# Kernel tuning notes

Hardware: AMD Instinct MI355X
Metric: run time of the kernel (lower is better)

Reference implementation:

```python
import jax, jax.numpy as jnp
import numpy as np

N, E, D, H, C = 50000, 1600000, 128, 2, 32

def setup_inputs() -> dict:
    key = jax.random.key(0)
    ks = jax.random.split(key, 8)
    x = jax.random.normal(ks[0], (N, D), jnp.float32)
    edge_index = jax.random.randint(ks[1], (2, E), 0, N)
    intra_enrichment_weights = jax.random.uniform(ks[2], (E,), jnp.float32)
    W = jax.random.normal(ks[3], (D, H * C), jnp.float32) * (1.0 / np.sqrt(D))
    att_src = jax.random.normal(ks[4], (H, C), jnp.float32) * 0.1
    att_dst = jax.random.normal(ks[5], (H, C), jnp.float32) * 0.1
    bias = jnp.zeros((H * C,), jnp.float32)
    enrichment_scale = jnp.asarray(0.01, jnp.float32)
    return dict(x=x, edge_index=edge_index,
                intra_enrichment_weights=intra_enrichment_weights,
                W=W, att_src=att_src, att_dst=att_dst, bias=bias,
                enrichment_scale=enrichment_scale)

def reference(x, edge_index, intra_enrichment_weights, W, att_src, att_dst, bias, enrichment_scale):
    n = x.shape[0]
    xf = jax.nn.elu(x)                       # F.elu on input features
    h = (xf @ W).reshape(n, H, C)            # [N, heads, out]
    # GATConv default add_self_loops=True
    loop = jnp.arange(n, dtype=edge_index.dtype)
    src = jnp.concatenate([edge_index[0], loop])
    dst = jnp.concatenate([edge_index[1], loop])
    a_src = jnp.einsum('nhc,hc->nh', h, att_src)   # [N, H]
    a_dst = jnp.einsum('nhc,hc->nh', h, att_dst)
    alpha = jax.nn.leaky_relu(a_src[src] + a_dst[dst], 0.2)  # [E+N, H]
    # softmax over incoming edges per destination node
    m = jax.ops.segment_max(alpha, dst, num_segments=n)
    e = jnp.exp(alpha - m[dst])
    denom = jax.ops.segment_sum(e, dst, num_segments=n)
    p = e / denom[dst]                       # every node has a self-loop -> denom > 0
    out = jax.ops.segment_sum(h[src] * p[:, :, None], dst, num_segments=n)  # [N, H, C]
    out = out.reshape(n, H * C) + bias
    # enrichment bias (scatter-mean of per-edge weights over source nodes)
    s0 = edge_index[0]
    nw = jax.ops.segment_sum(intra_enrichment_weights, s0, num_segments=n)
    cnt = jax.ops.segment_sum(jnp.ones_like(intra_enrichment_weights), s0, num_segments=n)
    nw = nw / jnp.maximum(cnt, 1.0)
    nw = jnp.clip(nw, 0.2, 5.0)
    scale_factor = 0.1 * jax.nn.sigmoid(enrichment_scale)
    return out + scale_factor * (nw[:, None] - 1.0)
```

## Files before the change

### kernel.cpp

```cpp
#include <hip/hip_runtime.h>


typedef unsigned int u32;
typedef unsigned short u16;

#define SLOTS2 2624
#define NB2_MAX 800
#define EPB 4096

#define XS 136
#define CS 68

#define SMEM_F 34816

typedef __attribute__((ext_vector_type(8))) short short8;
typedef __attribute__((ext_vector_type(4))) float float4v;

__device__ __forceinline__ u16 f2bf(float f) {
    union { float f; u32 u; } v; v.f = f;
    u32 r = v.u + 0x7fffu + ((v.u >> 16) & 1u);
    return (u16)(r >> 16);
}
__device__ __forceinline__ float bf2f(u16 u) {
    union { u32 i; float f; } v; v.i = ((u32)u) << 16; return v.f;
}
__device__ __forceinline__ float bf_lo(u32 u) {
    union { u32 i; float f; } v; v.i = u << 16; return v.f;
}
__device__ __forceinline__ float bf_hi(u32 u) {
    union { u32 i; float f; } v; v.i = u & 0xFFFF0000u; return v.f;
}
__device__ __forceinline__ void bf_split(float v, short& hi, short& lo) {
    u16 h = f2bf(v);
    float hf = bf2f(h);
    hi = (short)h;
    lo = (short)f2bf(v - hf);
}

__global__ void k_prep(const float* __restrict__ Wm,
                       short* __restrict__ Whf, short* __restrict__ Wlf,
                       int* cursA, int* cursB)
{
    int t = threadIdx.x;
    for (int i = t; i < NB2_MAX; i += 256) { cursA[i] = 0; cursB[i] = 0; }
    for (int p = t; p < 1024; p += 256) {
        int frag = p >> 6, l = p & 63;
        int ks = frag >> 2, nt = frag & 3;
        int q = l >> 4, m = l & 15;
        int f = nt * 16 + m;
#pragma unroll
        for (int j = 0; j < 8; ++j) {
            int k = ks * 32 + q * 8 + j;
            float wv = Wm[k * 64 + f];
            short hi, lo; bf_split(wv, hi, lo);
            Whf[p * 8 + j] = hi;
            Wlf[p * 8 + j] = lo;
        }
    }
}

static __device__ __forceinline__ void node_body(
    char* smem, int nb_id,
    const float* __restrict__ x,
    const short* __restrict__ Whf, const short* __restrict__ Wlf,
    const float* __restrict__ att_s, const float* __restrict__ att_d,
    u32* __restrict__ hb32, float* __restrict__ a_src, float* __restrict__ a_dst,
    int nN)
{
    short* Ah = (short*)smem;
    short* Al = (short*)(smem + 17408);
    float* Cl = (float*)Ah;

    int t = threadIdx.x;
    int n0 = nb_id * 64;

    for (int j = 0; j < 8; ++j) {
        int idx = t + 256 * j;
        int r = idx >> 5, c4 = idx & 31;
        int gn = n0 + r;
        float4 xv = make_float4(0.f, 0.f, 0.f, 0.f);
        if (gn < nN) xv = ((const float4*)x)[(size_t)gn * 32 + c4];
        float e[4];
        e[0] = xv.x > 0.f ? xv.x : __expf(xv.x) - 1.f;
        e[1] = xv.y > 0.f ? xv.y : __expf(xv.y) - 1.f;
        e[2] = xv.z > 0.f ? xv.z : __expf(xv.z) - 1.f;
        e[3] = xv.w > 0.f ? xv.w : __expf(xv.w) - 1.f;
        short h4[4], l4[4];
#pragma unroll
        for (int i = 0; i < 4; ++i) bf_split(e[i], h4[i], l4[i]);
        *(short4*)&Ah[r * XS + c4 * 4] = make_short4(h4[0], h4[1], h4[2], h4[3]);
        *(short4*)&Al[r * XS + c4 * 4] = make_short4(l4[0], l4[1], l4[2], l4[3]);
    }
    __syncthreads();

    {
        int w = t >> 6, l = t & 63;
        int q = l >> 4, m = l & 15;
        int arow = w * 16 + m;
        float4v acc[4] = {};
#pragma unroll
        for (int ks = 0; ks < 4; ++ks) {
            int k0 = ks * 32 + q * 8;
            short8 ah = *(const short8*)&Ah[arow * XS + k0];
            short8 al = *(const short8*)&Al[arow * XS + k0];
#pragma unroll
            for (int nt = 0; nt < 4; ++nt) {
                short8 bh = *(const short8*)&Whf[((ks * 4 + nt) * 64 + l) * 8];
                short8 bl = *(const short8*)&Wlf[((ks * 4 + nt) * 64 + l) * 8];
                acc[nt] = __builtin_amdgcn_mfma_f32_16x16x32_bf16(ah, bh, acc[nt], 0, 0, 0);
                acc[nt] = __builtin_amdgcn_mfma_f32_16x16x32_bf16(ah, bl, acc[nt], 0, 0, 0);
                acc[nt] = __builtin_amdgcn_mfma_f32_16x16x32_bf16(al, bh, acc[nt], 0, 0, 0);
            }
        }
        __syncthreads();
#pragma unroll
        for (int nt = 0; nt < 4; ++nt)
#pragma unroll
            for (int r = 0; r < 4; ++r)
                Cl[(w * 16 + q * 4 + r) * CS + nt * 16 + m] = acc[nt][r];
    }
    __syncthreads();

    {
        int nl = t >> 2, fq = t & 3;
        int gn = n0 + nl;
        float ps = 0.f, pd = 0.f;
        if (gn < nN) {
            float hv[16];
#pragma unroll
            for (int i = 0; i < 16; ++i) {
                int f = fq * 16 + i;
                hv[i] = Cl[nl * CS + f];
                ps = fmaf(hv[i], att_s[f], ps);
                pd = fmaf(hv[i], att_d[f], pd);
            }
#pragma unroll
            for (int i = 0; i < 8; ++i) {
                u32 pk = ((u32)f2bf(hv[2 * i + 1]) << 16) | (u32)f2bf(hv[2 * i]);
                hb32[(size_t)gn * 32 + fq * 8 + i] = pk;
            }
        }
        float ps2 = ps + __shfl_xor(ps, 1, 64);
        float pd2 = pd + __shfl_xor(pd, 1, 64);
        if (gn < nN && (fq & 1) == 0) {
            a_src[2 * gn + (fq >> 1)] = ps2;
            a_dst[2 * gn + (fq >> 1)] = pd2;
        }
    }
}

static __device__ __forceinline__ void sort_body(
    char* smem, int pa_id, int sideB,
    const int* __restrict__ ei, const float* __restrict__ wgt,
    int* curs, u32* buf, int E, int nb2)
{
    u32* arr  = (u32*)smem;
    int* cnt  = (int*)(smem + 16384);
    int* lofs = (int*)(smem + 19584);
    int* bas  = (int*)(smem + 22784);
    int* part = (int*)(smem + 25984);

    int t = threadIdx.x;
    int base = pa_id * EPB;
    int nv = min(EPB, E - base);
    int key[16]; u32 pay[16];
#pragma unroll
    for (int k = 0; k < 16; ++k) {
        int e = base + k * 256 + t;
        if (e < E) {
            if (sideB) {
                key[k] = ei[e];
                u32 wq = (u32)(wgt[e] * 65536.f);
                if (wq > 0xFFFFu) wq = 0xFFFFu;
                pay[k] = wq;
            } else {
                key[k] = ei[E + e];
                pay[k] = (u32)ei[e];
            }
        } else { key[k] = -1; pay[k] = 0u; }
    }

    for (int b = t; b < nb2; b += 256) cnt[b] = 0;
    __syncthreads();
#pragma unroll
    for (int k = 0; k < 16; ++k)
        if (key[k] >= 0) atomicAdd(&cnt[key[k] >> 6], 1);
    __syncthreads();
    for (int b = t; b < nb2; b += 256) {
        int c = cnt[b];
        if (c > 0) bas[b] = atomicAdd(&curs[b], c);
    }
    __syncthreads();
    {
        int c[4]; int s = 0;
#pragma unroll
        for (int i = 0; i < 4; ++i) {
            int bb = 4 * t + i;
            c[i] = (bb < nb2) ? cnt[bb] : 0;
            s += c[i];
        }
        part[t] = s;
        __syncthreads();
        for (int off = 1; off < 256; off <<= 1) {
            int v = (t >= off) ? part[t - off] : 0;
            __syncthreads();
            part[t] += v;
            __syncthreads();
        }
        int excl = part[t] - s;
#pragma unroll
        for (int i = 0; i < 4; ++i) {
            int bb = 4 * t + i;
            if (bb < nb2) lofs[bb] = excl;
            excl += c[i];
        }
    }
    __syncthreads();
    for (int b = t; b < nb2; b += 256) cnt[b] = 0;
    __syncthreads();
#pragma unroll
    for (int k = 0; k < 16; ++k) {
        if (key[k] >= 0) {
            int bk = key[k] >> 6;
            int r = lofs[bk] + atomicAdd(&cnt[bk], 1);
            arr[r] = ((u32)bk << 22) | ((u32)(key[k] & 63) << 16) | pay[k];
        }
    }
    __syncthreads();
    for (int i = t; i < nv; i += 256) {
        u32 va = arr[i];
        int bk = va >> 22;
        int g = bas[bk] + (i - lofs[bk]);
        if (g < SLOTS2) buf[(size_t)bk * SLOTS2 + g] = va & 0x3FFFFFu;
    }
}

__global__ __launch_bounds__(256) void k_fused(
    const float* __restrict__ x,
    const short* __restrict__ Whf, const short* __restrict__ Wlf,
    const float* __restrict__ att_s, const float* __restrict__ att_d,
    u32* __restrict__ hb32, float* __restrict__ a_src, float* __restrict__ a_dst,
    const int* __restrict__ ei, const float* __restrict__ wgt,
    int* cursA, int* cursB, u32* bufA, u32* bufB,
    int E, int nb2, int nblkA, int nN)
{
    __shared__ __align__(16) char smem[SMEM_F];
    int bid = blockIdx.x;
    int g = bid >> 2, r = bid & 3;
    if (g < nblkA && r == 0) {
        sort_body(smem, g, 0, ei, wgt, cursA, bufA, E, nb2);
    } else if (g < nblkA && r == 2) {
        sort_body(smem, g, 1, ei, wgt, cursB, bufB, E, nb2);
    } else {
        int sortBefore = (g < nblkA) ? (2 * g + (r >= 1 ? 1 : 0) + (r >= 3 ? 1 : 0))
                                     : 2 * nblkA;
        node_body(smem, bid - sortBefore, x, Whf, Wlf, att_s, att_d,
                  hb32, a_src, a_dst, nN);
    }
}

__global__ __launch_bounds__(512) void k_final(
    const u32* __restrict__ hb32,
    const float* __restrict__ a_src, const float* __restrict__ a_dst,
    const u32* __restrict__ bufA, const int* __restrict__ cursA,
    const u32* __restrict__ bufB, const int* __restrict__ cursB,
    const float* __restrict__ bias, const float* __restrict__ esc,
    float* __restrict__ out, int nN)
{
    __shared__ u32 st[SLOTS2];
    __shared__ u16 st2[SLOTS2];
    __shared__ int ldeg[64], lscan[64], lcur[64];
    __shared__ int usum[64], ucnt[64];

    int b = blockIdx.x, t = threadIdx.x;
    int n0 = b << 6;
    int nA = cursA[b]; if (nA > SLOTS2) nA = SLOTS2;
    int nB = cursB[b]; if (nB > SLOTS2) nB = SLOTS2;

    if (t < 64) { ldeg[t] = 0; lcur[t] = 0; usum[t] = 0; ucnt[t] = 0; }
    __syncthreads();
    for (int i = t; i < nA; i += 512) {
        u32 v = bufA[(size_t)b * SLOTS2 + i];
        st[i] = v;
        atomicAdd(&ldeg[v >> 16], 1);
    }
    for (int i = t; i < nB; i += 512) {
        u32 v = bufB[(size_t)b * SLOTS2 + i];
        atomicAdd(&usum[v >> 16], (int)(v & 0xFFFFu));
        atomicAdd(&ucnt[v >> 16], 1);
    }
    __syncthreads();
    if (t < 64) lscan[t] = ldeg[t];
    __syncthreads();
    for (int off = 1; off < 64; off <<= 1) {
        int v = 0;
        if (t < 64 && t >= off) v = lscan[t - off];
        __syncthreads();
        if (t < 64) lscan[t] += v;
        __syncthreads();
    }
    if (t < 64) lscan[t] -= ldeg[t];
    __syncthreads();
    for (int i = t; i < nA; i += 512) {
        u32 v = st[i];
        int dl = v >> 16;
        int pos = lscan[dl] + atomicAdd(&lcur[dl], 1);
        st2[pos] = (u16)(v & 0xFFFFu);
    }
    __syncthreads();

    int ws = t >> 6, lane = t & 63;
    int q = lane >> 4, fl = lane & 15, head = fl >> 3;
    const uint2* hb2 = (const uint2*)hb32;
    float escv = esc[0];
    float sf = 0.1f / (1.f + __expf(-escv));
    float4 bb = ((const float4*)bias)[fl];

    for (int dl0 = ws; dl0 < 64; dl0 += 16) {
        int dlA = dl0, dlB = dl0 + 8;
        int gnA = n0 + dlA, gnB = n0 + dlB;
        if (gnA >= nN) break;
        bool vB = (gnB < nN);

        int begA = lscan[dlA], cntA = ldeg[dlA];
        float2 advA = ((const float2*)a_dst)[gnA];
        float2 asvA = ((const float2*)a_src)[gnA];
        float tA0 = asvA.x + advA.x; tA0 = tA0 > 0.f ? tA0 : 0.2f * tA0;
        float tA1 = asvA.y + advA.y; tA1 = tA1 > 0.f ? tA1 : 0.2f * tA1;
        float esA0 = __expf(tA0), esA1 = __expf(tA1);
        float aA0 = 0.f, aA1 = 0.f, aA2 = 0.f, aA3 = 0.f;
        if (q == 0) {
            float eself = head ? esA1 : esA0;
            uint2 hs = hb2[(size_t)gnA * 16 + fl];
            aA0 = eself * bf_lo(hs.x); aA1 = eself * bf_hi(hs.x);
            aA2 = eself * bf_lo(hs.y); aA3 = eself * bf_hi(hs.y);
        }
        float dsA = 0.f;

        int begB = 0, cntB = 0;
        float2 advB = make_float2(0.f, 0.f);
        float esB0 = 0.f, esB1 = 0.f;
        float aB0 = 0.f, aB1 = 0.f, aB2 = 0.f, aB3 = 0.f;
        float dsB = 0.f;
        if (vB) {
            begB = lscan[dlB]; cntB = ldeg[dlB];
            advB = ((const float2*)a_dst)[gnB];
            float2 asvB = ((const float2*)a_src)[gnB];
            float tB0 = asvB.x + advB.x; tB0 = tB0 > 0.f ? tB0 : 0.2f * tB0;
            float tB1 = asvB.y + advB.y; tB1 = tB1 > 0.f ? tB1 : 0.2f * tB1;
            esB0 = __expf(tB0); esB1 = __expf(tB1);
            if (q == 0) {
                float eself = head ? esB1 : esB0;
                uint2 hs = hb2[(size_t)gnB * 16 + fl];
                aB0 = eself * bf_lo(hs.x); aB1 = eself * bf_hi(hs.x);
                aB2 = eself * bf_lo(hs.y); aB3 = eself * bf_hi(hs.y);
            }
        }

        int nwA = (cntA + 63) >> 6, nwB = (cntB + 63) >> 6;
        int nwin = nwA > nwB ? nwA : nwB;
        for (int w = 0; w < nwin; ++w) {
            int b0 = w << 6;
            u32 siA = (u32)gnA; float eA0 = 0.f, eA1 = 0.f; int wnA = 0;
            if (w < nwA) {
                wnA = cntA - b0; if (wnA > 64) wnA = 64;
                if (lane < wnA) {
                    siA = (u32)st2[begA + b0 + lane];
                    float2 ap = ((const float2*)a_src)[siA];
                    float v0 = ap.x + advA.x; v0 = v0 > 0.f ? v0 : 0.2f * v0;
                    float v1 = ap.y + advA.y; v1 = v1 > 0.f ? v1 : 0.2f * v1;
                    eA0 = __expf(v0); eA1 = __expf(v1);
                }
            }
            u32 siB = (u32)gnA; float eB0 = 0.f, eB1 = 0.f; int wnB = 0;
            if (w < nwB) {
                wnB = cntB - b0; if (wnB > 64) wnB = 64;
                if (lane < wnB) {
                    siB = (u32)st2[begB + b0 + lane];
                    float2 ap = ((const float2*)a_src)[siB];
                    float v0 = ap.x + advB.x; v0 = v0 > 0.f ? v0 : 0.2f * v0;
                    float v1 = ap.y + advB.y; v1 = v1 > 0.f ? v1 : 0.2f * v1;
                    eB0 = __expf(v0); eB1 = __expf(v1);
                }
            }
            int wmax = wnA > wnB ? wnA : wnB;
            int iters = (wmax + 3) >> 2;
#pragma unroll 4
            for (int k = 0; k < iters; ++k) {
                int e = 4 * k + q;
                u32 rsiA = __shfl(siA, e, 64);
                u32 rsiB = __shfl(siB, e, 64);
                uint2 hvA = hb2[(size_t)rsiA * 16 + fl];
                uint2 hvB = hb2[(size_t)rsiB * 16 + fl];
                float w0A = __shfl(eA0, e, 64), w1A = __shfl(eA1, e, 64);
                float w0B = __shfl(eB0, e, 64), w1B = __shfl(eB1, e, 64);
                float wA = head ? w1A : w0A;
                float wB = head ? w1B : w0B;
                dsA += wA; dsB += wB;
                aA0 = fmaf(wA, bf_lo(hvA.x), aA0);
                aA1 = fmaf(wA, bf_hi(hvA.x), aA1);
                aA2 = fmaf(wA, bf_lo(hvA.y), aA2);
                aA3 = fmaf(wA, bf_hi(hvA.y), aA3);
                aB0 = fmaf(wB, bf_lo(hvB.x), aB0);
                aB1 = fmaf(wB, bf_hi(hvB.x), aB1);
                aB2 = fmaf(wB, bf_lo(hvB.y), aB2);
                aB3 = fmaf(wB, bf_hi(hvB.y), aB3);
            }
        }
        dsA += __shfl_xor(dsA, 16, 64); dsA += __shfl_xor(dsA, 32, 64);
        dsB += __shfl_xor(dsB, 16, 64); dsB += __shfl_xor(dsB, 32, 64);
        aA0 += __shfl_xor(aA0, 16, 64); aA0 += __shfl_xor(aA0, 32, 64);
        aA1 += __shfl_xor(aA1, 16, 64); aA1 += __shfl_xor(aA1, 32, 64);
        aA2 += __shfl_xor(aA2, 16, 64); aA2 += __shfl_xor(aA2, 32, 64);
        aA3 += __shfl_xor(aA3, 16, 64); aA3 += __shfl_xor(aA3, 32, 64);
        aB0 += __shfl_xor(aB0, 16, 64); aB0 += __shfl_xor(aB0, 32, 64);
        aB1 += __shfl_xor(aB1, 16, 64); aB1 += __shfl_xor(aB1, 32, 64);
        aB2 += __shfl_xor(aB2, 16, 64); aB2 += __shfl_xor(aB2, 32, 64);
        aB3 += __shfl_xor(aB3, 16, 64); aB3 += __shfl_xor(aB3, 32, 64);

        if (q == 0) {
            {
                float den = (head ? esA1 : esA0) + dsA;
                float inv = 1.f / den;
                float cntf = (float)ucnt[dlA];
                float nw = ((float)usum[dlA] * (1.f / 65536.f)) / fmaxf(cntf, 1.f);
                nw = fminf(fmaxf(nw, 0.2f), 5.f);
                float en = sf * (nw - 1.f);
                float4 o;
                o.x = aA0 * inv + bb.x + en;
                o.y = aA1 * inv + bb.y + en;
                o.z = aA2 * inv + bb.z + en;
                o.w = aA3 * inv + bb.w + en;
                ((float4*)out)[(size_t)gnA * 16 + fl] = o;
            }
            if (vB) {
                float den = (head ? esB1 : esB0) + dsB;
                float inv = 1.f / den;
                float cntf = (float)ucnt[dlB];
                float nw = ((float)usum[dlB] * (1.f / 65536.f)) / fmaxf(cntf, 1.f);
                nw = fminf(fmaxf(nw, 0.2f), 5.f);
                float en = sf * (nw - 1.f);
                float4 o;
                o.x = aB0 * inv + bb.x + en;
                o.y = aB1 * inv + bb.y + en;
                o.z = aB2 * inv + bb.z + en;
                o.w = aB3 * inv + bb.w + en;
                ((float4*)out)[(size_t)gnB * 16 + fl] = o;
            }
        }
    }
}

extern "C" void kernel_launch(void* const* d_in, const int* in_sizes, int n_in,
                              void* d_out, int out_size, void* d_ws, size_t ws_size,
                              hipStream_t stream)
{
    const float* x     = (const float*)d_in[0];
    const int*   ei    = (const int*)d_in[1];
    const float* wgt   = (const float*)d_in[2];
    const float* Wm    = (const float*)d_in[3];
    const float* att_s = (const float*)d_in[4];
    const float* att_d = (const float*)d_in[5];
    const float* bias  = (const float*)d_in[6];
    const float* esc   = (const float*)d_in[7];
    float* out = (float*)d_out;

    int nN = in_sizes[0] / 128;
    int E  = in_sizes[2];
    int NB2 = (nN + 63) / 64;

    char* p = (char*)d_ws;
    auto alloc = [&](size_t bytes) -> char* {
        char* r = p; p += (bytes + 255) & ~(size_t)255; return r;
    };
    u32*   hb32  = (u32*)  alloc((size_t)nN * 32 * 4);
    float* a_src = (float*)alloc((size_t)nN * 2 * 4);
    float* a_dst = (float*)alloc((size_t)nN * 2 * 4);
    short* Whf   = (short*)alloc(16 * 64 * 8 * 2);
    short* Wlf   = (short*)alloc(16 * 64 * 8 * 2);
    int*   cursA = (int*)  alloc(NB2_MAX * 4);
    int*   cursB = (int*)  alloc(NB2_MAX * 4);
    u32*   bufA  = (u32*)  alloc((size_t)NB2 * SLOTS2 * 4);
    u32*   bufB  = (u32*)  alloc((size_t)NB2 * SLOTS2 * 4);

    int nblkA = (E + EPB - 1) / EPB;
    int nblkN = (nN + 63) / 64;
    int nblkF = 2 * nblkA + nblkN;

    k_prep<<<dim3(1), dim3(256), 0, stream>>>(Wm, Whf, Wlf, cursA, cursB);
    k_fused<<<dim3(nblkF), dim3(256), 0, stream>>>(x, Whf, Wlf, att_s, att_d,
                                                   hb32, a_src, a_dst,
                                                   ei, wgt, cursA, cursB, bufA, bufB,
                                                   E, NB2, nblkA, nN);
    k_final<<<dim3(NB2), dim3(512), 0, stream>>>(hb32, a_src, a_dst, bufA, cursA,
                                                 bufB, cursB, bias, esc, out, nN);
}
```

Measured before the change: 170.4 us.

## Process four destination nodes per wave in final kernel and drop staging buffer

Each wave in the final aggregation kernel now interleaves four destination nodes instead of two, which puts more independent gathers in flight and hides memory latency. The shared-memory staging array is removed and the bucket buffer is re-read from global memory in the second pass, which cuts LDS usage. Launch bounds now request 6 blocks per CU. The wider interleave raises register pressure and does more wasted padded iterations when node degrees differ, and the second global read adds traffic.

```diff
diff --git a/kernel.cpp b/kernel.cpp
--- a/kernel.cpp
+++ b/kernel.cpp
@@ -259,7 +259,7 @@
     }
 }
 
-__global__ __launch_bounds__(512) void k_final(
+__global__ __launch_bounds__(512, 6) void k_final(
     const u32* __restrict__ hb32,
     const float* __restrict__ a_src, const float* __restrict__ a_dst,
     const u32* __restrict__ bufA, const int* __restrict__ cursA,
@@ -267,7 +267,6 @@
     const float* __restrict__ bias, const float* __restrict__ esc,
     float* __restrict__ out, int nN)
 {
-    __shared__ u32 st[SLOTS2];
     __shared__ u16 st2[SLOTS2];
     __shared__ int ldeg[64], lscan[64], lcur[64];
     __shared__ int usum[64], ucnt[64];
@@ -281,7 +280,6 @@
     __syncthreads();
     for (int i = t; i < nA; i += 512) {
         u32 v = bufA[(size_t)b * SLOTS2 + i];
-        st[i] = v;
         atomicAdd(&ldeg[v >> 16], 1);
     }
     for (int i = t; i < nB; i += 512) {
@@ -302,7 +300,7 @@
     if (t < 64) lscan[t] -= ldeg[t];
     __syncthreads();
     for (int i = t; i < nA; i += 512) {
-        u32 v = st[i];
+        u32 v = bufA[(size_t)b * SLOTS2 + i];
         int dl = v >> 16;
         int pos = lscan[dl] + atomicAdd(&lcur[dl], 1);
         st2[pos] = (u16)(v & 0xFFFFu);
@@ -316,136 +314,107 @@
     float sf = 0.1f / (1.f + __expf(-escv));
     float4 bb = ((const float4*)bias)[fl];
 
-    for (int dl0 = ws; dl0 < 64; dl0 += 16) {
-        int dlA = dl0, dlB = dl0 + 8;
-        int gnA = n0 + dlA, gnB = n0 + dlB;
-        if (gnA >= nN) break;
-        bool vB = (gnB < nN);
-
-        int begA = lscan[dlA], cntA = ldeg[dlA];
-        float2 advA = ((const float2*)a_dst)[gnA];
-        float2 asvA = ((const float2*)a_src)[gnA];
-        float tA0 = asvA.x + advA.x; tA0 = tA0 > 0.f ? tA0 : 0.2f * tA0;
-        float tA1 = asvA.y + advA.y; tA1 = tA1 > 0.f ? tA1 : 0.2f * tA1;
-        float esA0 = __expf(tA0), esA1 = __expf(tA1);
-        float aA0 = 0.f, aA1 = 0.f, aA2 = 0.f, aA3 = 0.f;
-        if (q == 0) {
-            float eself = head ? esA1 : esA0;
-            uint2 hs = hb2[(size_t)gnA * 16 + fl];
-            aA0 = eself * bf_lo(hs.x); aA1 = eself * bf_hi(hs.x);
-            aA2 = eself * bf_lo(hs.y); aA3 = eself * bf_hi(hs.y);
-        }
-        float dsA = 0.f;
-
-        int begB = 0, cntB = 0;
-        float2 advB = make_float2(0.f, 0.f);
-        float esB0 = 0.f, esB1 = 0.f;
-        float aB0 = 0.f, aB1 = 0.f, aB2 = 0.f, aB3 = 0.f;
-        float dsB = 0.f;
-        if (vB) {
-            begB = lscan[dlB]; cntB = ldeg[dlB];
-            advB = ((const float2*)a_dst)[gnB];
-            float2 asvB = ((const float2*)a_src)[gnB];
-            float tB0 = asvB.x + advB.x; tB0 = tB0 > 0.f ? tB0 : 0.2f * tB0;
-            float tB1 = asvB.y + advB.y; tB1 = tB1 > 0.f ? tB1 : 0.2f * tB1;
-            esB0 = __expf(tB0); esB1 = __expf(tB1);
-            if (q == 0) {
-                float eself = head ? esB1 : esB0;
-                uint2 hs = hb2[(size_t)gnB * 16 + fl];
-                aB0 = eself * bf_lo(hs.x); aB1 = eself * bf_hi(hs.x);
-                aB2 = eself * bf_lo(hs.y); aB3 = eself * bf_hi(hs.y);
-            }
-        }
-
-        int nwA = (cntA + 63) >> 6, nwB = (cntB + 63) >> 6;
-        int nwin = nwA > nwB ? nwA : nwB;
+    for (int j = 0; j < 2; ++j) {
+        int dlb = ws + 32 * j;
+        int gn4[4], beg4[4], cnt4[4];
+        float adx[4], ady[4], e0s[4], e1s[4], ds4[4];
+        float ac0[4], ac1[4], ac2[4], ac3[4];
+        bool val[4];
+#pragma unroll
+        for (int c = 0; c < 4; ++c) {
+            int dl = dlb + 8 * c;
+            int g = n0 + dl;
+            gn4[c] = g;
+            val[c] = (g < nN);
+            beg4[c] = lscan[dl];
+            cnt4[c] = val[c] ? ldeg[dl] : 0;
+            float2 adv = make_float2(0.f, 0.f), asv = make_float2(0.f, 0.f);
+            if (val[c]) {
+                adv = ((const float2*)a_dst)[g];
+                asv = ((const float2*)a_src)[g];
+            }
+            adx[c] = adv.x; ady[c] = adv.y;
+            float t0 = asv.x + adv.x; t0 = t0 > 0.f ? t0 : 0.2f * t0;
+            float t1 = asv.y + adv.y; t1 = t1 > 0.f ? t1 : 0.2f * t1;
+            e0s[c] = __expf(t0); e1s[c] = __expf(t1);
+            ac0[c] = ac1[c] = ac2[c] = ac3[c] = 0.f;
+            ds4[c] = 0.f;
+            if (q == 0 && val[c]) {
+                float eself = head ? e1s[c] : e0s[c];
+                uint2 hs = hb2[(size_t)g * 16 + fl];
+                ac0[c] = eself * bf_lo(hs.x);
+                ac1[c] = eself * bf_hi(hs.x);
+                ac2[c] = eself * bf_lo(hs.y);
+                ac3[c] = eself * bf_hi(hs.y);
+            }
+        }
+        int nwin = 0;
+#pragma unroll
+        for (int c = 0; c < 4; ++c) {
+            int nw = (cnt4[c] + 63) >> 6;
+            if (nw > nwin) nwin = nw;
+        }
         for (int w = 0; w < nwin; ++w) {
             int b0 = w << 6;
-            u32 siA = (u32)gnA; float eA0 = 0.f, eA1 = 0.f; int wnA = 0;
-            if (w < nwA) {
-                wnA = cntA - b0; if (wnA > 64) wnA = 64;
-                if (lane < wnA) {
-                    siA = (u32)st2[begA + b0 + lane];
-                    float2 ap = ((const float2*)a_src)[siA];
-                    float v0 = ap.x + advA.x; v0 = v0 > 0.f ? v0 : 0.2f * v0;
-                    float v1 = ap.y + advA.y; v1 = v1 > 0.f ? v1 : 0.2f * v1;
-                    eA0 = __expf(v0); eA1 = __expf(v1);
+            u32 si4[4]; float we0[4], we1[4]; int wn4[4];
+#pragma unroll
+            for (int c = 0; c < 4; ++c) {
+                si4[c] = (u32)n0; we0[c] = 0.f; we1[c] = 0.f; wn4[c] = 0;
+                if (b0 < cnt4[c]) {
+                    int wn = cnt4[c] - b0; if (wn > 64) wn = 64;
+                    wn4[c] = wn;
+                    if (lane < wn) {
+                        si4[c] = (u32)st2[beg4[c] + b0 + lane];
+                        float2 ap = ((const float2*)a_src)[si4[c]];
+                        float v0 = ap.x + adx[c]; v0 = v0 > 0.f ? v0 : 0.2f * v0;
+                        float v1 = ap.y + ady[c]; v1 = v1 > 0.f ? v1 : 0.2f * v1;
+                        we0[c] = __expf(v0); we1[c] = __expf(v1);
+                    }
                 }
             }
-            u32 siB = (u32)gnA; float eB0 = 0.f, eB1 = 0.f; int wnB = 0;
-            if (w < nwB) {
-                wnB = cntB - b0; if (wnB > 64) wnB = 64;
-                if (lane < wnB) {
-                    siB = (u32)st2[begB + b0 + lane];
-                    float2 ap = ((const float2*)a_src)[siB];
-                    float v0 = ap.x + advB.x; v0 = v0 > 0.f ? v0 : 0.2f * v0;
-                    float v1 = ap.y + advB.y; v1 = v1 > 0.f ? v1 : 0.2f * v1;
-                    eB0 = __expf(v0); eB1 = __expf(v1);
-                }
-            }
-            int wmax = wnA > wnB ? wnA : wnB;
+            int wmax = 0;
+#pragma unroll
+            for (int c = 0; c < 4; ++c) if (wn4[c] > wmax) wmax = wn4[c];
             int iters = (wmax + 3) >> 2;
-#pragma unroll 4
+#pragma unroll 2
             for (int k = 0; k < iters; ++k) {
                 int e = 4 * k + q;
-                u32 rsiA = __shfl(siA, e, 64);
-                u32 rsiB = __shfl(siB, e, 64);
-                uint2 hvA = hb2[(size_t)rsiA * 16 + fl];
-                uint2 hvB = hb2[(size_t)rsiB * 16 + fl];
-                float w0A = __shfl(eA0, e, 64), w1A = __shfl(eA1, e, 64);
-                float w0B = __shfl(eB0, e, 64), w1B = __shfl(eB1, e, 64);
-                float wA = head ? w1A : w0A;
-                float wB = head ? w1B : w0B;
-                dsA += wA; dsB += wB;
-                aA0 = fmaf(wA, bf_lo(hvA.x), aA0);
-                aA1 = fmaf(wA, bf_hi(hvA.x), aA1);
-                aA2 = fmaf(wA, bf_lo(hvA.y), aA2);
-                aA3 = fmaf(wA, bf_hi(hvA.y), aA3);
-                aB0 = fmaf(wB, bf_lo(hvB.x), aB0);
-                aB1 = fmaf(wB, bf_hi(hvB.x), aB1);
-                aB2 = fmaf(wB, bf_lo(hvB.y), aB2);
-                aB3 = fmaf(wB, bf_hi(hvB.y), aB3);
-            }
-        }
-        dsA += __shfl_xor(dsA, 16, 64); dsA += __shfl_xor(dsA, 32, 64);
-        dsB += __shfl_xor(dsB, 16, 64); dsB += __shfl_xor(dsB, 32, 64);
-        aA0 += __shfl_xor(aA0, 16, 64); aA0 += __shfl_xor(aA0, 32, 64);
-        aA1 += __shfl_xor(aA1, 16, 64); aA1 += __shfl_xor(aA1, 32, 64);
-        aA2 += __shfl_xor(aA2, 16, 64); aA2 += __shfl_xor(aA2, 32, 64);
-        aA3 += __shfl_xor(aA3, 16, 64); aA3 += __shfl_xor(aA3, 32, 64);
-        aB0 += __shfl_xor(aB0, 16, 64); aB0 += __shfl_xor(aB0, 32, 64);
-        aB1 += __shfl_xor(aB1, 16, 64); aB1 += __shfl_xor(aB1, 32, 64);
-        aB2 += __shfl_xor(aB2, 16, 64); aB2 += __shfl_xor(aB2, 32, 64);
-        aB3 += __shfl_xor(aB3, 16, 64); aB3 += __shfl_xor(aB3, 32, 64);
-
-        if (q == 0) {
-            {
-                float den = (head ? esA1 : esA0) + dsA;
+#pragma unroll
+                for (int c = 0; c < 4; ++c) {
+                    u32 rsi = __shfl(si4[c], e, 64);
+                    uint2 hv = hb2[(size_t)rsi * 16 + fl];
+                    float w0 = __shfl(we0[c], e, 64);
+                    float w1 = __shfl(we1[c], e, 64);
+                    float wv = head ? w1 : w0;
+                    ds4[c] += wv;
+                    ac0[c] = fmaf(wv, bf_lo(hv.x), ac0[c]);
+                    ac1[c] = fmaf(wv, bf_hi(hv.x), ac1[c]);
+                    ac2[c] = fmaf(wv, bf_lo(hv.y), ac2[c]);
+                    ac3[c] = fmaf(wv, bf_hi(hv.y), ac3[c]);
+                }
+            }
+        }
+#pragma unroll
+        for (int c = 0; c < 4; ++c) {
+            ds4[c] += __shfl_xor(ds4[c], 16, 64); ds4[c] += __shfl_xor(ds4[c], 32, 64);
+            ac0[c] += __shfl_xor(ac0[c], 16, 64); ac0[c] += __shfl_xor(ac0[c], 32, 64);
+            ac1[c] += __shfl_xor(ac1[c], 16, 64); ac1[c] += __shfl_xor(ac1[c], 32, 64);
+            ac2[c] += __shfl_xor(ac2[c], 16, 64); ac2[c] += __shfl_xor(ac2[c], 32, 64);
+            ac3[c] += __shfl_xor(ac3[c], 16, 64); ac3[c] += __shfl_xor(ac3[c], 32, 64);
+            if (q == 0 && val[c]) {
+                int dl = dlb + 8 * c;
+                float den = (head ? e1s[c] : e0s[c]) + ds4[c];
                 float inv = 1.f / den;
-                float cntf = (float)ucnt[dlA];
-                float nw = ((float)usum[dlA] * (1.f / 65536.f)) / fmaxf(cntf, 1.f);
+                float cntf = (float)ucnt[dl];
+                float nw = ((float)usum[dl] * (1.f / 65536.f)) / fmaxf(cntf, 1.f);
                 nw = fminf(fmaxf(nw, 0.2f), 5.f);
                 float en = sf * (nw - 1.f);
                 float4 o;
-                o.x = aA0 * inv + bb.x + en;
-                o.y = aA1 * inv + bb.y + en;
-                o.z = aA2 * inv + bb.z + en;
-                o.w = aA3 * inv + bb.w + en;
-                ((float4*)out)[(size_t)gnA * 16 + fl] = o;
-            }
-            if (vB) {
-                float den = (head ? esB1 : esB0) + dsB;
-                float inv = 1.f / den;
-                float cntf = (float)ucnt[dlB];
-                float nw = ((float)usum[dlB] * (1.f / 65536.f)) / fmaxf(cntf, 1.f);
-                nw = fminf(fmaxf(nw, 0.2f), 5.f);
-                float en = sf * (nw - 1.f);
-                float4 o;
-                o.x = aB0 * inv + bb.x + en;
-                o.y = aB1 * inv + bb.y + en;
-                o.z = aB2 * inv + bb.z + en;
-                o.w = aB3 * inv + bb.w + en;
-                ((float4*)out)[(size_t)gnB * 16 + fl] = o;
+                o.x = ac0[c] * inv + bb.x + en;
+                o.y = ac1[c] * inv + bb.y + en;
+                o.z = ac2[c] * inv + bb.z + en;
+                o.w = ac3[c] * inv + bb.w + en;
+                ((float4*)out)[(size_t)gn4[c] * 16 + fl] = o;
             }
         }
     }
```

Result: slower. 200.4 us (+17.6%).

## Fuse prep, sort/node and final stages into one cooperative persistent kernel

Applied to the files above, without the earlier changes.

Replaces the three separate launches with a single cooperative kernel sized to full occupancy. Grid-wide syncs separate the phases, and atomic work counters hand out virtual blocks dynamically. The final stage now runs with 256 threads and shared memory carved from the common buffer, with a different node-to-wave assignment. The aim is to remove launch gaps and kernel-boundary drains. In exchange it adds grid.sync costs, atomic work-fetch overhead and possibly lower occupancy for the final phase, and it keeps the old three-kernel path as a fallback.

```diff
diff --git a/kernel.cpp b/kernel.cpp
--- a/kernel.cpp
+++ b/kernel.cpp
@@ -1,5 +1,8 @@
 #include <hip/hip_runtime.h>
-
+#include <hip/hip_cooperative_groups.h>
+
+
+namespace cg = cooperative_groups;
 
 typedef unsigned int u32;
 typedef unsigned short u16;
@@ -35,28 +38,6 @@
     float hf = bf2f(h);
     hi = (short)h;
     lo = (short)f2bf(v - hf);
-}
-
-__global__ void k_prep(const float* __restrict__ Wm,
-                       short* __restrict__ Whf, short* __restrict__ Wlf,
-                       int* cursA, int* cursB)
-{
-    int t = threadIdx.x;
-    for (int i = t; i < NB2_MAX; i += 256) { cursA[i] = 0; cursB[i] = 0; }
-    for (int p = t; p < 1024; p += 256) {
-        int frag = p >> 6, l = p & 63;
-        int ks = frag >> 2, nt = frag & 3;
-        int q = l >> 4, m = l & 15;
-        int f = nt * 16 + m;
-#pragma unroll
-        for (int j = 0; j < 8; ++j) {
-            int k = ks * 32 + q * 8 + j;
-            float wv = Wm[k * 64 + f];
-            short hi, lo; bf_split(wv, hi, lo);
-            Whf[p * 8 + j] = hi;
-            Wlf[p * 8 + j] = lo;
-        }
-    }
 }
 
 static __device__ __forceinline__ void node_body(
@@ -235,56 +216,36 @@
     }
 }
 
-__global__ __launch_bounds__(256) void k_fused(
-    const float* __restrict__ x,
-    const short* __restrict__ Whf, const short* __restrict__ Wlf,
-    const float* __restrict__ att_s, const float* __restrict__ att_d,
-    u32* __restrict__ hb32, float* __restrict__ a_src, float* __restrict__ a_dst,
-    const int* __restrict__ ei, const float* __restrict__ wgt,
-    int* cursA, int* cursB, u32* bufA, u32* bufB,
-    int E, int nb2, int nblkA, int nN)
-{
-    __shared__ __align__(16) char smem[SMEM_F];
-    int bid = blockIdx.x;
-    int g = bid >> 2, r = bid & 3;
-    if (g < nblkA && r == 0) {
-        sort_body(smem, g, 0, ei, wgt, cursA, bufA, E, nb2);
-    } else if (g < nblkA && r == 2) {
-        sort_body(smem, g, 1, ei, wgt, cursB, bufB, E, nb2);
-    } else {
-        int sortBefore = (g < nblkA) ? (2 * g + (r >= 1 ? 1 : 0) + (r >= 3 ? 1 : 0))
-                                     : 2 * nblkA;
-        node_body(smem, bid - sortBefore, x, Whf, Wlf, att_s, att_d,
-                  hb32, a_src, a_dst, nN);
-    }
-}
-
-__global__ __launch_bounds__(512) void k_final(
+static __device__ __forceinline__ void final_body(
+    char* smem, int b,
     const u32* __restrict__ hb32,
     const float* __restrict__ a_src, const float* __restrict__ a_dst,
     const u32* __restrict__ bufA, const int* __restrict__ cursA,
     const u32* __restrict__ bufB, const int* __restrict__ cursB,
-    const float* __restrict__ bias, const float* __restrict__ esc,
+    const float* __restrict__ bias, float sf,
     float* __restrict__ out, int nN)
 {
-    __shared__ u32 st[SLOTS2];
-    __shared__ u16 st2[SLOTS2];
-    __shared__ int ldeg[64], lscan[64], lcur[64];
-    __shared__ int usum[64], ucnt[64];
-
-    int b = blockIdx.x, t = threadIdx.x;
+    u32* st   = (u32*)smem;
+    u16* st2  = (u16*)(smem + 10496);
+    int* ldeg = (int*)(smem + 15744);
+    int* lscan= (int*)(smem + 16000);
+    int* lcur = (int*)(smem + 16256);
+    int* usum = (int*)(smem + 16512);
+    int* ucnt = (int*)(smem + 16768);
+
+    int t = threadIdx.x;
     int n0 = b << 6;
     int nA = cursA[b]; if (nA > SLOTS2) nA = SLOTS2;
     int nB = cursB[b]; if (nB > SLOTS2) nB = SLOTS2;
 
     if (t < 64) { ldeg[t] = 0; lcur[t] = 0; usum[t] = 0; ucnt[t] = 0; }
     __syncthreads();
-    for (int i = t; i < nA; i += 512) {
+    for (int i = t; i < nA; i += 256) {
         u32 v = bufA[(size_t)b * SLOTS2 + i];
         st[i] = v;
         atomicAdd(&ldeg[v >> 16], 1);
     }
-    for (int i = t; i < nB; i += 512) {
+    for (int i = t; i < nB; i += 256) {
         u32 v = bufB[(size_t)b * SLOTS2 + i];
         atomicAdd(&usum[v >> 16], (int)(v & 0xFFFFu));
         atomicAdd(&ucnt[v >> 16], 1);
@@ -301,7 +262,7 @@
     }
     if (t < 64) lscan[t] -= ldeg[t];
     __syncthreads();
-    for (int i = t; i < nA; i += 512) {
+    for (int i = t; i < nA; i += 256) {
         u32 v = st[i];
         int dl = v >> 16;
         int pos = lscan[dl] + atomicAdd(&lcur[dl], 1);
@@ -312,12 +273,10 @@
     int ws = t >> 6, lane = t & 63;
     int q = lane >> 4, fl = lane & 15, head = fl >> 3;
     const uint2* hb2 = (const uint2*)hb32;
-    float escv = esc[0];
-    float sf = 0.1f / (1.f + __expf(-escv));
     float4 bb = ((const float4*)bias)[fl];
 
-    for (int dl0 = ws; dl0 < 64; dl0 += 16) {
-        int dlA = dl0, dlB = dl0 + 8;
+    for (int i4 = 0; i4 < 8; ++i4) {
+        int dlA = ws + 4 * i4, dlB = dlA + 32;
         int gnA = n0 + dlA, gnB = n0 + dlB;
         if (gnA >= nN) break;
         bool vB = (gnB < nN);
@@ -451,6 +410,137 @@
     }
 }
 
+__global__ __launch_bounds__(256, 4) void k_mega(
+    const float* __restrict__ x, const int* __restrict__ ei,
+    const float* __restrict__ wgt, const float* __restrict__ Wm,
+    const float* __restrict__ att_s, const float* __restrict__ att_d,
+    const float* __restrict__ bias, const float* __restrict__ esc,
+    float* __restrict__ out,
+    u32* hb32, float* a_src, float* a_dst, short* Whf, short* Wlf,
+    int* cursA, int* cursB, u32* bufA, u32* bufB, int* wctr,
+    int E, int nb2, int nblkA, int nblkF, int nN)
+{
+    __shared__ __align__(16) char smem[SMEM_F];
+    __shared__ int vb_sh;
+    cg::grid_group grid = cg::this_grid();
+    int bid = blockIdx.x, t = threadIdx.x;
+
+    for (int p = bid; p < 1024; p += gridDim.x) {
+        if (t < 8) {
+            int frag = p >> 6, l = p & 63;
+            int ks = frag >> 2, nt = frag & 3;
+            int qq = l >> 4, m = l & 15;
+            int f = nt * 16 + m;
+            int k = ks * 32 + qq * 8 + t;
+            float wv = Wm[k * 64 + f];
+            short hi, lo; bf_split(wv, hi, lo);
+            Whf[p * 8 + t] = hi;
+            Wlf[p * 8 + t] = lo;
+        }
+    }
+    if (bid == 0) {
+        for (int i = t; i < NB2_MAX; i += 256) { cursA[i] = 0; cursB[i] = 0; }
+        if (t < 2) wctr[t] = 0;
+    }
+    __threadfence();
+    grid.sync();
+
+    for (;;) {
+        if (t == 0) vb_sh = atomicAdd(&wctr[0], 1);
+        __syncthreads();
+        int vb = vb_sh;
+        if (vb >= nblkF) break;
+        int g = vb >> 2, r = vb & 3;
+        if (g < nblkA && r == 0) {
+            sort_body(smem, g, 0, ei, wgt, cursA, bufA, E, nb2);
+        } else if (g < nblkA && r == 2) {
+            sort_body(smem, g, 1, ei, wgt, cursB, bufB, E, nb2);
+        } else {
+            int sortBefore = (g < nblkA) ? (2 * g + (r >= 1 ? 1 : 0) + (r >= 3 ? 1 : 0))
+                                         : 2 * nblkA;
+            node_body(smem, vb - sortBefore, x, Whf, Wlf, att_s, att_d,
+                      hb32, a_src, a_dst, nN);
+        }
+        __syncthreads();
+    }
+    __threadfence();
+    grid.sync();
+
+    float escv = esc[0];
+    float sf = 0.1f / (1.f + __expf(-escv));
+    for (;;) {
+        if (t == 0) vb_sh = atomicAdd(&wctr[1], 1);
+        __syncthreads();
+        int b = vb_sh;
+        if (b >= nb2) break;
+        final_body(smem, b, hb32, a_src, a_dst, bufA, cursA, bufB, cursB,
+                   bias, sf, out, nN);
+        __syncthreads();
+    }
+}
+
+
+__global__ void k_prep(const float* __restrict__ Wm,
+                       short* __restrict__ Whf, short* __restrict__ Wlf,
+                       int* cursA, int* cursB)
+{
+    int t = threadIdx.x;
+    for (int i = t; i < NB2_MAX; i += 256) { cursA[i] = 0; cursB[i] = 0; }
+    for (int p = t; p < 1024; p += 256) {
+        int frag = p >> 6, l = p & 63;
+        int ks = frag >> 2, nt = frag & 3;
+        int q = l >> 4, m = l & 15;
+        int f = nt * 16 + m;
+#pragma unroll
+        for (int j = 0; j < 8; ++j) {
+            int k = ks * 32 + q * 8 + j;
+            float wv = Wm[k * 64 + f];
+            short hi, lo; bf_split(wv, hi, lo);
+            Whf[p * 8 + j] = hi;
+            Wlf[p * 8 + j] = lo;
+        }
+    }
+}
+
+__global__ __launch_bounds__(256) void k_fused(
+    const float* __restrict__ x,
+    const short* __restrict__ Whf, const short* __restrict__ Wlf,
+    const float* __restrict__ att_s, const float* __restrict__ att_d,
+    u32* __restrict__ hb32, float* __restrict__ a_src, float* __restrict__ a_dst,
+    const int* __restrict__ ei, const float* __restrict__ wgt,
+    int* cursA, int* cursB, u32* bufA, u32* bufB,
+    int E, int nb2, int nblkA, int nN)
+{
+    __shared__ __align__(16) char smem[SMEM_F];
+    int bid = blockIdx.x;
+    int g = bid >> 2, r = bid & 3;
+    if (g < nblkA && r == 0) {
+        sort_body(smem, g, 0, ei, wgt, cursA, bufA, E, nb2);
+    } else if (g < nblkA && r == 2) {
+        sort_body(smem, g, 1, ei, wgt, cursB, bufB, E, nb2);
+    } else {
+        int sortBefore = (g < nblkA) ? (2 * g + (r >= 1 ? 1 : 0) + (r >= 3 ? 1 : 0))
+                                     : 2 * nblkA;
+        node_body(smem, bid - sortBefore, x, Whf, Wlf, att_s, att_d,
+                  hb32, a_src, a_dst, nN);
+    }
+}
+
+__global__ __launch_bounds__(256) void k_final(
+    const u32* __restrict__ hb32,
+    const float* __restrict__ a_src, const float* __restrict__ a_dst,
+    const u32* __restrict__ bufA, const int* __restrict__ cursA,
+    const u32* __restrict__ bufB, const int* __restrict__ cursB,
+    const float* __restrict__ bias, const float* __restrict__ esc,
+    float* __restrict__ out, int nN)
+{
+    __shared__ __align__(16) char smem[SMEM_F];
+    float escv = esc[0];
+    float sf = 0.1f / (1.f + __expf(-escv));
+    final_body(smem, blockIdx.x, hb32, a_src, a_dst, bufA, cursA, bufB, cursB,
+               bias, sf, out, nN);
+}
+
 extern "C" void kernel_launch(void* const* d_in, const int* in_sizes, int n_in,
                               void* d_out, int out_size, void* d_ws, size_t ws_size,
                               hipStream_t stream)
@@ -480,6 +570,7 @@
     short* Wlf   = (short*)alloc(16 * 64 * 8 * 2);
     int*   cursA = (int*)  alloc(NB2_MAX * 4);
     int*   cursB = (int*)  alloc(NB2_MAX * 4);
+    int*   wctr  = (int*)  alloc(256);
     u32*   bufA  = (u32*)  alloc((size_t)NB2 * SLOTS2 * 4);
     u32*   bufB  = (u32*)  alloc((size_t)NB2 * SLOTS2 * 4);
 
@@ -487,11 +578,36 @@
     int nblkN = (nN + 63) / 64;
     int nblkF = 2 * nblkA + nblkN;
 
-    k_prep<<<dim3(1), dim3(256), 0, stream>>>(Wm, Whf, Wlf, cursA, cursB);
-    k_fused<<<dim3(nblkF), dim3(256), 0, stream>>>(x, Whf, Wlf, att_s, att_d,
-                                                   hb32, a_src, a_dst,
-                                                   ei, wgt, cursA, cursB, bufA, bufB,
-                                                   E, NB2, nblkA, nN);
-    k_final<<<dim3(NB2), dim3(512), 0, stream>>>(hb32, a_src, a_dst, bufA, cursA,
-                                                 bufB, cursB, bias, esc, out, nN);
-}
+    static int coopGrid = -2;
+    if (coopGrid == -2) {
+        int nb = 0, cus = 0, dev = 0;
+        hipError_t e0 = hipGetDevice(&dev);
+        hipError_t e1 = hipOccupancyMaxActiveBlocksPerMultiprocessor(&nb, k_mega, 256, 0);
+        hipError_t e2 = hipDeviceGetAttribute(&cus, hipDeviceAttributeMultiprocessorCount, dev);
+        coopGrid = (e0 == hipSuccess && e1 == hipSuccess && e2 == hipSuccess &&
+                    nb > 0 && cus > 0) ? nb * cus : -1;
+    }
+
+    bool launched = false;
+    if (coopGrid > 0) {
+        void* args[] = { (void*)&x, (void*)&ei, (void*)&wgt, (void*)&Wm,
+                         (void*)&att_s, (void*)&att_d, (void*)&bias, (void*)&esc,
+                         (void*)&out, (void*)&hb32, (void*)&a_src, (void*)&a_dst,
+                         (void*)&Whf, (void*)&Wlf, (void*)&cursA, (void*)&cursB,
+                         (void*)&bufA, (void*)&bufB, (void*)&wctr,
+                         (void*)&E, (void*)&NB2, (void*)&nblkA, (void*)&nblkF,
+                         (void*)&nN };
+        if (hipLaunchCooperativeKernel(k_mega, dim3(coopGrid), dim3(256),
+                                       args, 0, stream) == hipSuccess)
+            launched = true;
+    }
+    if (!launched) {
+        k_prep<<<dim3(1), dim3(256), 0, stream>>>(Wm, Whf, Wlf, cursA, cursB);
+        k_fused<<<dim3(nblkF), dim3(256), 0, stream>>>(x, Whf, Wlf, att_s, att_d,
+                                                       hb32, a_src, a_dst,
+                                                       ei, wgt, cursA, cursB, bufA, bufB,
+                                                       E, NB2, nblkA, nN);
+        k_final<<<dim3(NB2), dim3(256), 0, stream>>>(hb32, a_src, a_dst, bufA, cursA,
+                                                     bufB, cursB, bias, esc, out, nN);
+    }
+}
```

After: 493.1 us. 189% more time.

## Split each final-aggregation bucket across two 256-thread blocks of 32 nodes

Applied to the files above, without the earlier changes.

The final kernel now launches two 256-thread blocks per 64-node bucket, and each block handles only the 32 destination nodes of its half. Both blocks still read the whole bucket buffer and keep only the entries for their half. This doubles the block count so the grid fills more of the GPU and the per-block load is better balanced. The cost is that every bucket's edge list is read and scanned twice, which adds redundant global loads and filtering work.

```diff
diff --git a/kernel.cpp b/kernel.cpp
--- a/kernel.cpp
+++ b/kernel.cpp
@@ -259,7 +259,7 @@
     }
 }
 
-__global__ __launch_bounds__(512) void k_final(
+__global__ __launch_bounds__(256) void k_final(
     const u32* __restrict__ hb32,
     const float* __restrict__ a_src, const float* __restrict__ a_dst,
     const u32* __restrict__ bufA, const int* __restrict__ cursA,
@@ -269,43 +269,50 @@
 {
     __shared__ u32 st[SLOTS2];
     __shared__ u16 st2[SLOTS2];
-    __shared__ int ldeg[64], lscan[64], lcur[64];
-    __shared__ int usum[64], ucnt[64];
-
-    int b = blockIdx.x, t = threadIdx.x;
-    int n0 = b << 6;
-    int nA = cursA[b]; if (nA > SLOTS2) nA = SLOTS2;
-    int nB = cursB[b]; if (nB > SLOTS2) nB = SLOTS2;
-
-    if (t < 64) { ldeg[t] = 0; lcur[t] = 0; usum[t] = 0; ucnt[t] = 0; }
-    __syncthreads();
-    for (int i = t; i < nA; i += 512) {
-        u32 v = bufA[(size_t)b * SLOTS2 + i];
+    __shared__ int ldeg[32], lscan[32], lcur[32];
+    __shared__ int usum[32], ucnt[32];
+
+    int bc = blockIdx.x >> 1, half = blockIdx.x & 1;
+    int t = threadIdx.x;
+    int n0 = (bc << 6) + (half << 5);
+    int nA = cursA[bc]; if (nA > SLOTS2) nA = SLOTS2;
+    int nB = cursB[bc]; if (nB > SLOTS2) nB = SLOTS2;
+
+    if (t < 32) { ldeg[t] = 0; lcur[t] = 0; usum[t] = 0; ucnt[t] = 0; }
+    __syncthreads();
+    for (int i = t; i < nA; i += 256) {
+        u32 v = bufA[(size_t)bc * SLOTS2 + i];
         st[i] = v;
-        atomicAdd(&ldeg[v >> 16], 1);
-    }
-    for (int i = t; i < nB; i += 512) {
-        u32 v = bufB[(size_t)b * SLOTS2 + i];
-        atomicAdd(&usum[v >> 16], (int)(v & 0xFFFFu));
-        atomicAdd(&ucnt[v >> 16], 1);
-    }
-    __syncthreads();
-    if (t < 64) lscan[t] = ldeg[t];
-    __syncthreads();
-    for (int off = 1; off < 64; off <<= 1) {
+        int dl = v >> 16;
+        if ((dl >> 5) == half) atomicAdd(&ldeg[dl & 31], 1);
+    }
+    for (int i = t; i < nB; i += 256) {
+        u32 v = bufB[(size_t)bc * SLOTS2 + i];
+        int sl = v >> 16;
+        if ((sl >> 5) == half) {
+            atomicAdd(&usum[sl & 31], (int)(v & 0xFFFFu));
+            atomicAdd(&ucnt[sl & 31], 1);
+        }
+    }
+    __syncthreads();
+    if (t < 32) lscan[t] = ldeg[t];
+    __syncthreads();
+    for (int off = 1; off < 32; off <<= 1) {
         int v = 0;
-        if (t < 64 && t >= off) v = lscan[t - off];
+        if (t < 32 && t >= off) v = lscan[t - off];
         __syncthreads();
-        if (t < 64) lscan[t] += v;
+        if (t < 32) lscan[t] += v;
         __syncthreads();
     }
-    if (t < 64) lscan[t] -= ldeg[t];
-    __syncthreads();
-    for (int i = t; i < nA; i += 512) {
+    if (t < 32) lscan[t] -= ldeg[t];
+    __syncthreads();
+    for (int i = t; i < nA; i += 256) {
         u32 v = st[i];
         int dl = v >> 16;
-        int pos = lscan[dl] + atomicAdd(&lcur[dl], 1);
-        st2[pos] = (u16)(v & 0xFFFFu);
+        if ((dl >> 5) == half) {
+            int pos = lscan[dl & 31] + atomicAdd(&lcur[dl & 31], 1);
+            st2[pos] = (u16)(v & 0xFFFFu);
+        }
     }
     __syncthreads();
 
@@ -316,8 +323,8 @@
     float sf = 0.1f / (1.f + __expf(-escv));
     float4 bb = ((const float4*)bias)[fl];
 
-    for (int dl0 = ws; dl0 < 64; dl0 += 16) {
-        int dlA = dl0, dlB = dl0 + 8;
+    for (int i4 = 0; i4 < 4; ++i4) {
+        int dlA = ws + 4 * i4, dlB = dlA + 16;
         int gnA = n0 + dlA, gnB = n0 + dlB;
         if (gnA >= nN) break;
         bool vB = (gnB < nN);
@@ -492,6 +499,6 @@
                                                    hb32, a_src, a_dst,
                                                    ei, wgt, cursA, cursB, bufA, bufB,
                                                    E, NB2, nblkA, nN);
-    k_final<<<dim3(NB2), dim3(512), 0, stream>>>(hb32, a_src, a_dst, bufA, cursA,
-                                                 bufB, cursB, bias, esc, out, nN);
-}
+    k_final<<<dim3(NB2 * 2), dim3(256), 0, stream>>>(hb32, a_src, a_dst, bufA, cursA,
+                                                     bufB, cursB, bias, esc, out, nN);
+}
```

Result: no change. 173.5 us (+1.8%).
